# Kernel optimization log

Hardware: AMD Instinct MI355X
Metric: run time of the kernel (lower is better)

The kernel has to match this reference:

```python
import jax, jax.numpy as jnp
import numpy as np

E = 8          # num_global_experts
K = 2          # top-k
D = 1024       # model_dim
H = 4096       # hidden_size_per_expert
CAP_FACTOR = 1.0


def setup_inputs() -> dict:
    key = jax.random.key(0)
    ks = jax.random.split(key, 5)
    x = jax.random.normal(ks[0], (4, 2048, D), jnp.float32)
    gate_w = jax.random.normal(ks[1], (E, D), jnp.float32) * 0.02
    fc1_w = jax.random.normal(ks[2], (E, H, D), jnp.float32) * 0.02
    fc1_b = jnp.zeros((E, 1, H), jnp.float32)
    fc2_w = jax.random.normal(ks[3], (E, H, D), jnp.float32) * 0.02
    fc2_b = jnp.zeros((E, 1, D), jnp.float32)
    return {"x": x, "gate_w": gate_w, "fc1_w": fc1_w, "fc1_b": fc1_b,
            "fc2_w": fc2_w, "fc2_b": fc2_b}


def reference(x, gate_w, fc1_w, fc1_b, fc2_w, fc2_b):
    B, S, Dm = x.shape
    xf = x.reshape(-1, Dm)                       # [N, D] tokens
    N = xf.shape[0]
    cap = int(K * CAP_FACTOR * ((N + E - 1) // E))  # expert capacity

    # ---- gating (top-k softmax, normalized) ----
    logits = xf @ gate_w.T                       # [N, E]
    scores = jax.nn.softmax(logits, axis=-1)
    topv, topi = jax.lax.top_k(scores, K)        # [N, K]
    gates = topv / jnp.sum(topv, axis=-1, keepdims=True)

    # ---- per-slot locations within each expert (sequential over K slots) ----
    offset = jnp.zeros((E,), jnp.int32)
    locs = []
    for j in range(K):
        mask = jax.nn.one_hot(topi[:, j], E, dtype=jnp.int32)   # [N, E]
        loc_in = jnp.cumsum(mask, axis=0) - 1 + offset[None, :]
        locs.append(jnp.take_along_axis(loc_in, topi[:, j:j + 1], axis=1)[:, 0])
        offset = offset + mask.sum(axis=0)
    loc = jnp.stack(locs, axis=1)                # [N, K]
    valid = loc < cap                            # capacity-dropped tokens
    flat_idx = jnp.where(valid, topi * cap + loc, 0)   # [N, K]
    w = valid.astype(xf.dtype)

    # ---- dispatch (scatter tokens into [E, cap, D], postscore => unweighted) ----
    disp = jnp.zeros((E * cap, Dm), xf.dtype)
    disp = disp.at[flat_idx.reshape(-1)].add(
        (xf[:, None, :] * w[:, :, None]).reshape(-1, Dm))
    de = disp.reshape(E, cap, Dm)

    # ---- batched expert FFN: relu(x @ fc1^T + b1) @ fc2 + b2 ----
    h = jax.nn.relu(jnp.einsum('ecd,ehd->ech', de, fc1_w) + fc1_b)
    eo = jnp.einsum('ech,ehd->ecd', h, fc2_w) + fc2_b

    # ---- combine (gather + gate-weighted sum over K slots) ----
    gathered = eo.reshape(E * cap, Dm)[flat_idx]       # [N, K, D]
    out = jnp.sum(gathered * (gates * w)[:, :, None], axis=1)
    return out.reshape(B, S, Dm)
```

## Files before the change

### kernel.cpp

```cpp
#include <hip/hip_runtime.h>
#include <hip/hip_bf16.h>
#include <stdint.h>

#define NEXP 8
#define DM   1024
#define HID  4096
#define NTOK 8192
#define CAPS 2048

#define BM 256
#define BN 256
#define BK 64

typedef __attribute__((ext_vector_type(8))) short bh8_t;
typedef __attribute__((ext_vector_type(4))) float f32x4_t;
typedef unsigned short u16;

static __device__ __forceinline__ u16 f2bf(float f) {
    __hip_bfloat16 h = __float2bfloat16(f);
    return __builtin_bit_cast(u16, h);
}
static __device__ __forceinline__ float bf2f(u16 u) {
    unsigned int x = ((unsigned int)u) << 16;
    return __builtin_bit_cast(float, x);
}

#define FENCE asm volatile("" ::: "memory")
#define BAR   do { FENCE; __builtin_amdgcn_s_barrier(); FENCE; } while (0)
#define MFMA(d, a, b) d = __builtin_amdgcn_mfma_f32_16x16x32_bf16(a, b, d, 0, 0, 0)
#define WAITVM(n) do { if ((n) == 4) asm volatile("s_waitcnt vmcnt(4)" ::: "memory"); \
    else if ((n) == 0) asm volatile("s_waitcnt vmcnt(0)" ::: "memory"); } while (0)

__global__ __launch_bounds__(256) void k_conv_bf16(const float* __restrict__ in,
                                                   u16* __restrict__ out, long n4) {
    long stride = (long)gridDim.x * 256;
    for (long i = (long)blockIdx.x * 256 + threadIdx.x; i < n4; i += stride) {
        float4 v = ((const float4*)in)[i];
        ushort4 o;
        o.x = f2bf(v.x); o.y = f2bf(v.y); o.z = f2bf(v.z); o.w = f2bf(v.w);
        ((ushort4*)out)[i] = o;
    }
}

__global__ __launch_bounds__(256) void k_transpose_w2(const float* __restrict__ in,
                                                      u16* __restrict__ out) {
    int e = blockIdx.z;
    const float* I = in + (long)e * HID * DM;
    u16* O = out + (long)e * DM * HID;
    __shared__ float t[64][65];
    int h0 = blockIdx.x * 64, d0 = blockIdx.y * 64;
    int tid = threadIdx.x;
    int r = tid >> 4, cw = (tid & 15) * 4;
    #pragma unroll
    for (int i = 0; i < 4; ++i) {
        float4 v = *(const float4*)(I + (long)(h0 + r + 16*i) * DM + d0 + cw);
        t[r + 16*i][cw]     = v.x;
        t[r + 16*i][cw + 1] = v.y;
        t[r + 16*i][cw + 2] = v.z;
        t[r + 16*i][cw + 3] = v.w;
    }
    __syncthreads();
    int dl = tid >> 2, hc = (tid & 3) * 16;
    bh8_t w0, w1;
    #pragma unroll
    for (int j = 0; j < 8; ++j) w0[j] = (short)f2bf(t[hc + j][dl]);
    #pragma unroll
    for (int j = 0; j < 8; ++j) w1[j] = (short)f2bf(t[hc + 8 + j][dl]);
    u16* o = O + (long)(d0 + dl) * HID + h0 + hc;
    *(bh8_t*)o = w0;
    *(bh8_t*)(o + 8) = w1;
}

__global__ __launch_bounds__(256) void k_gating(const float* __restrict__ x,
        const float* __restrict__ gw, int* __restrict__ topi, float* __restrict__ gates) {
    __shared__ float sg[NEXP][DM];
    int tid = threadIdx.x;
    for (int i = tid; i < NEXP*DM; i += 256) ((float*)sg)[i] = gw[i];
    __syncthreads();
    int lane = tid & 63, w = tid >> 6;
    long n = (long)blockIdx.x * 4 + w;
    const float* xr = x + n * DM;
    float acc[NEXP] = {};
    for (int i = 0; i < DM/64; ++i) {
        float xv = xr[lane + i*64];
        #pragma unroll
        for (int e = 0; e < NEXP; ++e) acc[e] += xv * sg[e][lane + i*64];
    }
    #pragma unroll
    for (int e = 0; e < NEXP; ++e)
        #pragma unroll
        for (int off = 32; off; off >>= 1) acc[e] += __shfl_xor(acc[e], off);
    if (lane == 0) {
        float mx = acc[0];
        #pragma unroll
        for (int e = 1; e < NEXP; ++e) mx = fmaxf(mx, acc[e]);
        float p[NEXP];
        #pragma unroll
        for (int e = 0; e < NEXP; ++e) p[e] = expf(acc[e] - mx);
        float v0 = p[0]; int i0 = 0;
        #pragma unroll
        for (int e = 1; e < NEXP; ++e) if (p[e] > v0) { v0 = p[e]; i0 = e; }
        float v1 = -1.f; int i1 = 0;
        #pragma unroll
        for (int e = 0; e < NEXP; ++e) if (e != i0 && p[e] > v1) { v1 = p[e]; i1 = e; }
        float tot = v0 + v1;
        topi[n*2]   = i0; topi[n*2+1] = i1;
        gates[n*2]  = v0 / tot; gates[n*2+1] = v1 / tot;
    }
}

__global__ __launch_bounds__(256) void k_locate(const int* __restrict__ topi,
                                                int* __restrict__ flat) {
    __shared__ int st[NTOK * 2];
    __shared__ int wsum[4];
    int e = blockIdx.x;
    int tid = threadIdx.x, lane = tid & 63, w = tid >> 6;
    int4* st4 = (int4*)st;
    const int4* g4 = (const int4*)topi;
    for (int i = tid; i < NTOK * 2 / 4; i += 256) st4[i] = g4[i];
    __syncthreads();
    const int TPL = NTOK / 256;
    int base = tid * TPL;
    int offset = 0;
    for (int j = 0; j < 2; ++j) {
        int cnt = 0;
        for (int t = 0; t < TPL; ++t) cnt += (st[(base + t) * 2 + j] == e);
        int v = cnt;
        #pragma unroll
        for (int d = 1; d < 64; d <<= 1) {
            int o = __shfl_up(v, d);
            if (lane >= d) v += o;
        }
        if (lane == 63) wsum[w] = v;
        __syncthreads();
        int wb = 0;
        #pragma unroll
        for (int ww = 0; ww < 4; ++ww) if (ww < w) wb += wsum[ww];
        int tot = wsum[0] + wsum[1] + wsum[2] + wsum[3];
        int loc = v - cnt + wb + offset;
        offset += tot;
        for (int t = 0; t < TPL; ++t) {
            int n = base + t;
            if (st[n * 2 + j] == e) {
                flat[n * 2 + j] = (loc < CAPS) ? (e * CAPS + loc) : -1;
                ++loc;
            }
        }
        __syncthreads();
    }
}

__global__ __launch_bounds__(256) void k_dispatch(const float* __restrict__ x,
        const int* __restrict__ flat, u16* __restrict__ disp) {
    long n = blockIdx.x;
    int tid = threadIdx.x;
    float4 v = *(const float4*)(x + n*DM + tid*4);
    ushort4 o; o.x = f2bf(v.x); o.y = f2bf(v.y); o.z = f2bf(v.z); o.w = f2bf(v.w);
    int f0 = flat[n*2], f1 = flat[n*2+1];
    if (f0 >= 0) *(ushort4*)(disp + (long)f0*DM + tid*4) = o;
    if (f1 >= 0) *(ushort4*)(disp + (long)f1*DM + tid*4) = o;
}

static __device__ __forceinline__ void stage_half(const u16* __restrict__ g, int ld,
                                                  u16* R, int wid, int lane) {
    int rlo = wid*8 + (lane >> 3);
    int cbe = ((lane & 7) ^ ((lane >> 3) & 7)) * 8;
    const u16* s0 = g + (long)rlo * ld + cbe;
    const u16* s1 = g + (long)(rlo + 64) * ld + cbe;
    u16* d0 = R + wid*512 + lane*8;
    u16* d1 = R + 4096 + wid*512 + lane*8;
    __builtin_amdgcn_global_load_lds((const __attribute__((address_space(1))) void*)s0,
        (__attribute__((address_space(3))) void*)d0, 16, 0, 0);
    __builtin_amdgcn_global_load_lds((const __attribute__((address_space(1))) void*)s1,
        (__attribute__((address_space(3))) void*)d1, 16, 0, 0);
}

template<int RELU>
__global__ __launch_bounds__(512, 2)
void k_gemm8(const u16* __restrict__ A, const u16* __restrict__ B,
             const float* __restrict__ bias, u16* __restrict__ C,
             int N, int K, long strA, long strB, long strBias, long strC)
{
    __shared__ u16 sm[2][2][2][8192];

    int gx = gridDim.x, gy = gridDim.y;
    int nwg = gx * gy * (int)gridDim.z;
    int lin = blockIdx.x + gx * (blockIdx.y + gy * blockIdx.z);
    int qq  = nwg >> 3;
    int swz = (lin & 7) * qq + (lin >> 3);
    int gxy = gx * gy;
    int bz = swz / gxy, rm = swz % gxy, by = rm / gx, bx = rm % gx;

    const float* bi = bias + (long)bz * strBias;
    u16* Ce = C + (long)bz * strC;

    long tm = (long)by * BM, tn = (long)bx * BN;
    const u16* Abase = A + (long)bz * strA + tm * (long)K;
    const u16* Bbase = B + (long)bz * strB + tn * (long)K;

    int tid = threadIdx.x, lane = tid & 63, wid = tid >> 6;
    int wr = wid >> 2, wc = wid & 3;

    int frow = lane & 15;
    int fc0 = (((lane >> 4) * 16)      ^ ((lane & 7) << 4)) >> 1;
    int fc1 = ((64 + (lane >> 4) * 16) ^ ((lane & 7) << 4)) >> 1;

    const int NT = K / BK;

    f32x4_t acc[8][4] = {};

    auto STG = [&](int buf, int ab, int half, int kt) {
        const u16* g = (ab ? Bbase : Abase) + (long)(half * 128) * K + (long)kt * BK;
        stage_half(g, K, &sm[buf][ab][half][0], wid, lane);
    };
    auto LDA = [&](int c, int half, int mi, int kk) -> bh8_t {
        const u16* p = &sm[c][0][half][0] + (wr * 64 + mi * 16 + frow) * 64 + (kk ? fc1 : fc0);
        return *(const bh8_t*)p;
    };
    auto LDB = [&](int c, int half, int ni, int kk) -> bh8_t {
        const u16* p = &sm[c][1][half][0] + (wc * 32 + ni * 16 + frow) * 64 + (kk ? fc1 : fc0);
        return *(const bh8_t*)p;
    };

    auto ktile = [&](int c, int kt, int s12, int s34, int vmexit) {
        bh8_t a0[4][2], a1[4][2], b0[2][2], b1[2][2];
        #pragma unroll
        for (int mi = 0; mi < 4; ++mi) { a0[mi][0] = LDA(c, 0, mi, 0); a0[mi][1] = LDA(c, 0, mi, 1); }
        #pragma unroll
        for (int ni = 0; ni < 2; ++ni) { b0[ni][0] = LDB(c, 0, ni, 0); b0[ni][1] = LDB(c, 0, ni, 1); }
        if (s12) STG(c ^ 1, 1, 1, kt + 1);
        __builtin_amdgcn_s_setprio(1);
        #pragma unroll
        for (int mi = 0; mi < 4; ++mi)
            #pragma unroll
            for (int ni = 0; ni < 2; ++ni)
                #pragma unroll
                for (int kk = 0; kk < 2; ++kk) MFMA(acc[mi][ni], a0[mi][kk], b0[ni][kk]);
        __builtin_amdgcn_s_setprio(0);
        #pragma unroll
        for (int ni = 0; ni < 2; ++ni) { b1[ni][0] = LDB(c, 1, ni, 0); b1[ni][1] = LDB(c, 1, ni, 1); }
        if (s12) STG(c ^ 1, 0, 1, kt + 1);
        __builtin_amdgcn_s_setprio(1);
        #pragma unroll
        for (int mi = 0; mi < 4; ++mi)
            #pragma unroll
            for (int ni = 0; ni < 2; ++ni)
                #pragma unroll
                for (int kk = 0; kk < 2; ++kk) MFMA(acc[mi][2 + ni], a0[mi][kk], b1[ni][kk]);
        __builtin_amdgcn_s_setprio(0);
        BAR;
        #pragma unroll
        for (int mi = 0; mi < 4; ++mi) { a1[mi][0] = LDA(c, 1, mi, 0); a1[mi][1] = LDA(c, 1, mi, 1); }
        if (s34) STG(c, 0, 0, kt + 2);
        __builtin_amdgcn_s_setprio(1);
        #pragma unroll
        for (int mi = 0; mi < 4; ++mi)
            #pragma unroll
            for (int ni = 0; ni < 2; ++ni)
                #pragma unroll
                for (int kk = 0; kk < 2; ++kk) MFMA(acc[4 + mi][ni], a1[mi][kk], b0[ni][kk]);
        __builtin_amdgcn_s_setprio(0);
        if (s34) STG(c, 1, 0, kt + 2);
        __builtin_amdgcn_s_setprio(1);
        #pragma unroll
        for (int mi = 0; mi < 4; ++mi)
            #pragma unroll
            for (int ni = 0; ni < 2; ++ni)
                #pragma unroll
                for (int kk = 0; kk < 2; ++kk) MFMA(acc[4 + mi][2 + ni], a1[mi][kk], b1[ni][kk]);
        __builtin_amdgcn_s_setprio(0);
        WAITVM(vmexit);
        BAR;
    };

    STG(0, 0, 0, 0); STG(0, 1, 0, 0); STG(0, 1, 1, 0); STG(0, 0, 1, 0);
    STG(1, 0, 0, 1); STG(1, 1, 0, 1);
    asm volatile("s_waitcnt vmcnt(4)" ::: "memory");
    BAR;

    int kt = 0;
    for (; kt < NT - 2; ++kt) ktile(kt & 1, kt, 1, 1, 4);
    ktile(kt & 1, kt, 1, 0, 0); ++kt;
    ktile(kt & 1, kt, 0, 0, -1);

    u16* wb = &sm[0][0][0][0] + wid * 8192;
    #pragma unroll
    for (int mi = 0; mi < 8; ++mi)
        #pragma unroll
        for (int ni = 0; ni < 4; ++ni) {
            float bv = bi[tn + (ni >> 1) * 128 + wc * 32 + (ni & 1) * 16 + (lane & 15)];
            #pragma unroll
            for (int r = 0; r < 4; ++r) {
                int row = mi * 16 + (lane >> 4) * 4 + r;
                int ce  = ni * 16 + (lane & 15);
                float v = acc[mi][ni][r] + bv;
                if (RELU) v = fmaxf(v, 0.f);
                wb[row * 64 + (ce ^ ((row & 7) << 3))] = f2bf(v);
            }
        }
    __syncthreads();
    long crow0 = tm + wr * 64;
    long ccol  = tn + wc * 32 + (lane & 3) * 8 + ((lane >> 2) & 1) * 128;
    #pragma unroll
    for (int i = 0; i < 16; ++i) {
        int rr = i * 8 + (lane >> 3);
        bh8_t v = *(const bh8_t*)(wb + rr * 64 + (((lane & 7) * 8) ^ ((rr & 7) << 3)));
        long grow = crow0 + (rr & 63) + (rr >> 6) * 128;
        *(bh8_t*)(Ce + grow * N + ccol) = v;
    }
}

__global__ __launch_bounds__(256) void k_combine(const u16* __restrict__ eo,
        const int* __restrict__ flat, const float* __restrict__ gates,
        float* __restrict__ out) {
    long n = blockIdx.x;
    int tid = threadIdx.x;
    int f0 = flat[n*2], f1 = flat[n*2+1];
    float g0 = (f0 >= 0) ? gates[n*2]   : 0.f;
    float g1 = (f1 >= 0) ? gates[n*2+1] : 0.f;
    const u16* r0 = eo + (long)(f0 >= 0 ? f0 : 0) * DM;
    const u16* r1 = eo + (long)(f1 >= 0 ? f1 : 0) * DM;
    ushort4 a = *(const ushort4*)(r0 + tid*4);
    ushort4 b = *(const ushort4*)(r1 + tid*4);
    float4 o;
    o.x = g0*bf2f(a.x) + g1*bf2f(b.x);
    o.y = g0*bf2f(a.y) + g1*bf2f(b.y);
    o.z = g0*bf2f(a.z) + g1*bf2f(b.z);
    o.w = g0*bf2f(a.w) + g1*bf2f(b.w);
    *(float4*)(out + n*DM + tid*4) = o;
}

extern "C" void kernel_launch(void* const* d_in, const int* in_sizes, int n_in,
                              void* d_out, int out_size, void* d_ws, size_t ws_size,
                              hipStream_t stream) {
    const float* x    = (const float*)d_in[0];
    const float* gw   = (const float*)d_in[1];
    const float* fc1w = (const float*)d_in[2];
    const float* fc1b = (const float*)d_in[3];
    const float* fc2w = (const float*)d_in[4];
    const float* fc2b = (const float*)d_in[5];
    float* out = (float*)d_out;
    char* ws = (char*)d_ws;

    u16* disp = (u16*)(ws);
    u16* eo   = disp;
    u16* h    = (u16*)(ws + 33554432L);
    u16* w1b  = (u16*)(ws + 33554432L + 134217728L);
    u16* w2t  = (u16*)(ws + 33554432L + 134217728L + 67108864L);
    char* tail = ws + 33554432L + 134217728L + 67108864L + 67108864L;
    int*   topi  = (int*)tail;
    float* gates = (float*)(tail + 65536);
    int*   flat  = (int*)(tail + 131072);

    long n1 = (long)NEXP * HID * DM;

    k_conv_bf16<<<dim3(2048), 256, 0, stream>>>(fc1w, w1b, n1 / 4);
    k_transpose_w2<<<dim3(HID/64, DM/64, NEXP), 256, 0, stream>>>(fc2w, w2t);
    k_gating<<<dim3(NTOK/4), 256, 0, stream>>>(x, gw, topi, gates);
    k_locate<<<dim3(NEXP), 256, 0, stream>>>(topi, flat);
    k_dispatch<<<dim3(NTOK), 256, 0, stream>>>(x, flat, disp);
    k_gemm8<1><<<dim3(HID/BN, CAPS/BM, NEXP), 512, 0, stream>>>(
        disp, w1b, fc1b, h, HID, DM,
        (long)CAPS*DM, (long)HID*DM, (long)HID, (long)CAPS*HID);
    k_gemm8<0><<<dim3(DM/BN, CAPS/BM, NEXP), 512, 0, stream>>>(
        h, w2t, fc2b, eo, DM, HID,
        (long)CAPS*HID, (long)DM*HID, (long)DM, (long)CAPS*DM);
    k_combine<<<dim3(NTOK), 256, 0, stream>>>(eo, flat, gates, out);
}
```

Baseline: 382.0 us.

## Shrink GEMM tile to 256x128x32 with simpler pipeline and higher occupancy

Rewrites the expert GEMM kernel to use a 256x128 output tile with BK=32 instead of 256x256x64. Each wave now owns a 64x64 sub-tile with 16 accumulators instead of 32, and LDS use drops to 48 KB. Launch bounds rise from 2 to 4 blocks per CU. The staging, LDS swizzle and epilogue are restructured to match, and the epilogue writes through LDS in two passes. The aim is more resident waves and more blocks to hide latency, at the cost of less operand reuse per tile and more barriers per unit of work.

```diff
diff --git a/kernel.cpp b/kernel.cpp
--- a/kernel.cpp
+++ b/kernel.cpp
@@ -9,8 +9,8 @@
 #define CAPS 2048
 
 #define BM 256
-#define BN 256
-#define BK 64
+#define BN 128
+#define BK 32
 
 typedef __attribute__((ext_vector_type(8))) short bh8_t;
 typedef __attribute__((ext_vector_type(4))) float f32x4_t;
@@ -28,8 +28,11 @@
 #define FENCE asm volatile("" ::: "memory")
 #define BAR   do { FENCE; __builtin_amdgcn_s_barrier(); FENCE; } while (0)
 #define MFMA(d, a, b) d = __builtin_amdgcn_mfma_f32_16x16x32_bf16(a, b, d, 0, 0, 0)
-#define WAITVM(n) do { if ((n) == 4) asm volatile("s_waitcnt vmcnt(4)" ::: "memory"); \
+#define WAITVM(n) do { if ((n) == 3) asm volatile("s_waitcnt vmcnt(3)" ::: "memory"); \
     else if ((n) == 0) asm volatile("s_waitcnt vmcnt(0)" ::: "memory"); } while (0)
+#define GLD(p, d) __builtin_amdgcn_global_load_lds( \
+    (const __attribute__((address_space(1))) void*)(p), \
+    (__attribute__((address_space(3))) void*)(d), 16, 0, 0)
 
 __global__ __launch_bounds__(256) void k_conv_bf16(const float* __restrict__ in,
                                                    u16* __restrict__ out, long n4) {
@@ -161,27 +164,13 @@
     if (f1 >= 0) *(ushort4*)(disp + (long)f1*DM + tid*4) = o;
 }
 
-static __device__ __forceinline__ void stage_half(const u16* __restrict__ g, int ld,
-                                                  u16* R, int wid, int lane) {
-    int rlo = wid*8 + (lane >> 3);
-    int cbe = ((lane & 7) ^ ((lane >> 3) & 7)) * 8;
-    const u16* s0 = g + (long)rlo * ld + cbe;
-    const u16* s1 = g + (long)(rlo + 64) * ld + cbe;
-    u16* d0 = R + wid*512 + lane*8;
-    u16* d1 = R + 4096 + wid*512 + lane*8;
-    __builtin_amdgcn_global_load_lds((const __attribute__((address_space(1))) void*)s0,
-        (__attribute__((address_space(3))) void*)d0, 16, 0, 0);
-    __builtin_amdgcn_global_load_lds((const __attribute__((address_space(1))) void*)s1,
-        (__attribute__((address_space(3))) void*)d1, 16, 0, 0);
-}
-
 template<int RELU>
-__global__ __launch_bounds__(512, 2)
+__global__ __launch_bounds__(512, 4)
 void k_gemm8(const u16* __restrict__ A, const u16* __restrict__ B,
              const float* __restrict__ bias, u16* __restrict__ C,
              int N, int K, long strA, long strB, long strBias, long strC)
 {
-    __shared__ u16 sm[2][2][2][8192];
+    __shared__ u16 sm[2][12288];
 
     int gx = gridDim.x, gy = gridDim.y;
     int nwg = gx * gy * (int)gridDim.z;
@@ -199,114 +188,98 @@
     const u16* Bbase = B + (long)bz * strB + tn * (long)K;
 
     int tid = threadIdx.x, lane = tid & 63, wid = tid >> 6;
-    int wr = wid >> 2, wc = wid & 3;
+    int wr = wid >> 1, wc = wid & 1;
 
     int frow = lane & 15;
-    int fc0 = (((lane >> 4) * 16)      ^ ((lane & 7) << 4)) >> 1;
-    int fc1 = ((64 + (lane >> 4) * 16) ^ ((lane & 7) << 4)) >> 1;
+    int fcs = (((lane >> 4) ^ ((frow >> 1) & 3)) * 8);
+
+    int srow = tid >> 2;
+    int scol = ((tid & 3) ^ ((tid >> 3) & 3)) * 8;
+    int sdst = tid * 8;
 
     const int NT = K / BK;
 
-    f32x4_t acc[8][4] = {};
-
-    auto STG = [&](int buf, int ab, int half, int kt) {
-        const u16* g = (ab ? Bbase : Abase) + (long)(half * 128) * K + (long)kt * BK;
-        stage_half(g, K, &sm[buf][ab][half][0], wid, lane);
-    };
-    auto LDA = [&](int c, int half, int mi, int kk) -> bh8_t {
-        const u16* p = &sm[c][0][half][0] + (wr * 64 + mi * 16 + frow) * 64 + (kk ? fc1 : fc0);
-        return *(const bh8_t*)p;
-    };
-    auto LDB = [&](int c, int half, int ni, int kk) -> bh8_t {
-        const u16* p = &sm[c][1][half][0] + (wc * 32 + ni * 16 + frow) * 64 + (kk ? fc1 : fc0);
-        return *(const bh8_t*)p;
-    };
-
-    auto ktile = [&](int c, int kt, int s12, int s34, int vmexit) {
-        bh8_t a0[4][2], a1[4][2], b0[2][2], b1[2][2];
-        #pragma unroll
-        for (int mi = 0; mi < 4; ++mi) { a0[mi][0] = LDA(c, 0, mi, 0); a0[mi][1] = LDA(c, 0, mi, 1); }
-        #pragma unroll
-        for (int ni = 0; ni < 2; ++ni) { b0[ni][0] = LDB(c, 0, ni, 0); b0[ni][1] = LDB(c, 0, ni, 1); }
-        if (s12) STG(c ^ 1, 1, 1, kt + 1);
+    f32x4_t acc[4][4] = {};
+
+    auto STGA = [&](int buf, int kt) {
+        const u16* g = Abase + (long)kt * BK + (long)srow * K + scol;
+        u16* R = &sm[buf][0] + sdst;
+        GLD(g, R);
+        GLD(g + 128L * K, R + 4096);
+    };
+    auto STGB = [&](int buf, int kt) {
+        const u16* g = Bbase + (long)kt * BK + (long)srow * K + scol;
+        GLD(g, &sm[buf][8192] + sdst);
+    };
+    auto LDA = [&](int c, int mi) -> bh8_t {
+        return *(const bh8_t*)(&sm[c][0] + (wr * 64 + mi * 16 + frow) * 32 + fcs);
+    };
+    auto LDB = [&](int c, int ni) -> bh8_t {
+        return *(const bh8_t*)(&sm[c][8192] + (wc * 64 + ni * 16 + frow) * 32 + fcs);
+    };
+
+    auto ktile = [&](int c, int kt, int s1, int s2, int vmexit) {
+        bh8_t a[4], b[4];
+        #pragma unroll
+        for (int mi = 0; mi < 4; ++mi) a[mi] = LDA(c, mi);
+        #pragma unroll
+        for (int ni = 0; ni < 4; ++ni) b[ni] = LDB(c, ni);
+        if (s1) { STGB(c ^ 1, kt + 1); STGA(c ^ 1, kt + 1); }
         __builtin_amdgcn_s_setprio(1);
         #pragma unroll
         for (int mi = 0; mi < 4; ++mi)
             #pragma unroll
-            for (int ni = 0; ni < 2; ++ni)
-                #pragma unroll
-                for (int kk = 0; kk < 2; ++kk) MFMA(acc[mi][ni], a0[mi][kk], b0[ni][kk]);
+            for (int ni = 0; ni < 2; ++ni) MFMA(acc[mi][ni], a[mi], b[ni]);
         __builtin_amdgcn_s_setprio(0);
-        #pragma unroll
-        for (int ni = 0; ni < 2; ++ni) { b1[ni][0] = LDB(c, 1, ni, 0); b1[ni][1] = LDB(c, 1, ni, 1); }
-        if (s12) STG(c ^ 1, 0, 1, kt + 1);
+        BAR;
+        if (s2) { STGB(c, kt + 2); STGA(c, kt + 2); }
         __builtin_amdgcn_s_setprio(1);
         #pragma unroll
         for (int mi = 0; mi < 4; ++mi)
             #pragma unroll
-            for (int ni = 0; ni < 2; ++ni)
-                #pragma unroll
-                for (int kk = 0; kk < 2; ++kk) MFMA(acc[mi][2 + ni], a0[mi][kk], b1[ni][kk]);
-        __builtin_amdgcn_s_setprio(0);
-        BAR;
-        #pragma unroll
-        for (int mi = 0; mi < 4; ++mi) { a1[mi][0] = LDA(c, 1, mi, 0); a1[mi][1] = LDA(c, 1, mi, 1); }
-        if (s34) STG(c, 0, 0, kt + 2);
-        __builtin_amdgcn_s_setprio(1);
-        #pragma unroll
-        for (int mi = 0; mi < 4; ++mi)
-            #pragma unroll
-            for (int ni = 0; ni < 2; ++ni)
-                #pragma unroll
-                for (int kk = 0; kk < 2; ++kk) MFMA(acc[4 + mi][ni], a1[mi][kk], b0[ni][kk]);
-        __builtin_amdgcn_s_setprio(0);
-        if (s34) STG(c, 1, 0, kt + 2);
-        __builtin_amdgcn_s_setprio(1);
-        #pragma unroll
-        for (int mi = 0; mi < 4; ++mi)
-            #pragma unroll
-            for (int ni = 0; ni < 2; ++ni)
-                #pragma unroll
-                for (int kk = 0; kk < 2; ++kk) MFMA(acc[4 + mi][2 + ni], a1[mi][kk], b1[ni][kk]);
+            for (int ni = 2; ni < 4; ++ni) MFMA(acc[mi][ni], a[mi], b[ni]);
         __builtin_amdgcn_s_setprio(0);
         WAITVM(vmexit);
         BAR;
     };
 
-    STG(0, 0, 0, 0); STG(0, 1, 0, 0); STG(0, 1, 1, 0); STG(0, 0, 1, 0);
-    STG(1, 0, 0, 1); STG(1, 1, 0, 1);
-    asm volatile("s_waitcnt vmcnt(4)" ::: "memory");
+    STGB(0, 0); STGA(0, 0);
+    STGB(1, 1); STGA(1, 1);
+    asm volatile("s_waitcnt vmcnt(3)" ::: "memory");
     BAR;
 
     int kt = 0;
-    for (; kt < NT - 2; ++kt) ktile(kt & 1, kt, 1, 1, 4);
+    for (; kt < NT - 2; ++kt) ktile(kt & 1, kt, 1, 1, 3);
     ktile(kt & 1, kt, 1, 0, 0); ++kt;
     ktile(kt & 1, kt, 0, 0, -1);
 
-    u16* wb = &sm[0][0][0][0] + wid * 8192;
-    #pragma unroll
-    for (int mi = 0; mi < 8; ++mi)
-        #pragma unroll
-        for (int ni = 0; ni < 4; ++ni) {
-            float bv = bi[tn + (ni >> 1) * 128 + wc * 32 + (ni & 1) * 16 + (lane & 15)];
+    u16* wb = &sm[0][0] + wid * 2048;
+    #pragma unroll
+    for (int p = 0; p < 2; ++p) {
+        #pragma unroll
+        for (int m2 = 0; m2 < 2; ++m2) {
+            int mi = p * 2 + m2;
             #pragma unroll
-            for (int r = 0; r < 4; ++r) {
-                int row = mi * 16 + (lane >> 4) * 4 + r;
-                int ce  = ni * 16 + (lane & 15);
-                float v = acc[mi][ni][r] + bv;
-                if (RELU) v = fmaxf(v, 0.f);
-                wb[row * 64 + (ce ^ ((row & 7) << 3))] = f2bf(v);
+            for (int ni = 0; ni < 4; ++ni) {
+                float bv = bi[tn + wc * 64 + ni * 16 + (lane & 15)];
+                #pragma unroll
+                for (int r = 0; r < 4; ++r) {
+                    int row = m2 * 16 + (lane >> 4) * 4 + r;
+                    int ce  = ni * 16 + (lane & 15);
+                    float v = acc[mi][ni][r] + bv;
+                    if (RELU) v = fmaxf(v, 0.f);
+                    wb[row * 64 + (ce ^ ((row & 7) << 3))] = f2bf(v);
+                }
             }
         }
-    __syncthreads();
-    long crow0 = tm + wr * 64;
-    long ccol  = tn + wc * 32 + (lane & 3) * 8 + ((lane >> 2) & 1) * 128;
-    #pragma unroll
-    for (int i = 0; i < 16; ++i) {
-        int rr = i * 8 + (lane >> 3);
-        bh8_t v = *(const bh8_t*)(wb + rr * 64 + (((lane & 7) * 8) ^ ((rr & 7) << 3)));
-        long grow = crow0 + (rr & 63) + (rr >> 6) * 128;
-        *(bh8_t*)(Ce + grow * N + ccol) = v;
+        #pragma unroll
+        for (int i = 0; i < 4; ++i) {
+            int rr = i * 8 + (lane >> 3);
+            bh8_t v = *(const bh8_t*)(wb + rr * 64 + (((lane & 7) * 8) ^ ((rr & 7) << 3)));
+            long grow = tm + wr * 64 + p * 32 + rr;
+            long gcol = tn + wc * 64 + (lane & 7) * 8;
+            *(bh8_t*)(Ce + grow * N + gcol) = v;
+        }
     }
 }
 
```

New measurement: 575.4 us. +50.6%, slower.
